# Kernel optimization log

Hardware: AMD Instinct MI355X
Metric: run time of the kernel (lower is better)

## Reference

```python
import jax, jax.numpy as jnp
import numpy as np

B, N, E = 8, 2000, 32000
LAT, STY, NF = 128, 64, 10
HEADS, HID = 4, 128
OUT = 3 + NF  # 13
EPS = 1e-5
SLOPE = 0.2


def _lin(k, fi, fo):
    return jax.random.normal(k, (fi, fo), dtype=jnp.float32) / np.sqrt(fi)


def setup_inputs() -> dict:
    key = jax.random.key(0)
    ks = jax.random.split(key, 32)
    inp = {
        'z': jax.random.normal(ks[0], (B, LAT), dtype=jnp.float32),
        'template_x': jax.random.normal(ks[1], (N, NF), dtype=jnp.float32),
        'template_edge_index': jax.random.randint(ks[2], (2, E), 0, N, dtype=jnp.int32),
        # style MLP
        'mlp_w1': _lin(ks[3], LAT, 256), 'mlp_b1': jnp.zeros((256,), jnp.float32),
        'mlp_w2': _lin(ks[4], 256, 512), 'mlp_b2': jnp.zeros((512,), jnp.float32),
        'mlp_w3': _lin(ks[5], 512, STY), 'mlp_b3': jnp.zeros((STY,), jnp.float32),
        # GAT1: in = NF + STY = 74 -> heads*HID = 512, concat
        'gat1_w': _lin(ks[6], NF + STY, HEADS * HID),
        'gat1_as': jax.random.normal(ks[7], (HEADS, HID), jnp.float32) * 0.1,
        'gat1_ad': jax.random.normal(ks[8], (HEADS, HID), jnp.float32) * 0.1,
        'gat1_b': jnp.zeros((HEADS * HID,), jnp.float32),
        'ln1_g': jnp.ones((HEADS * HID,), jnp.float32), 'ln1_b': jnp.zeros((HEADS * HID,), jnp.float32),
        # GAT2: 512 -> 512, concat
        'gat2_w': _lin(ks[9], HEADS * HID, HEADS * HID),
        'gat2_as': jax.random.normal(ks[10], (HEADS, HID), jnp.float32) * 0.1,
        'gat2_ad': jax.random.normal(ks[11], (HEADS, HID), jnp.float32) * 0.1,
        'gat2_b': jnp.zeros((HEADS * HID,), jnp.float32),
        'ln2_g': jnp.ones((HEADS * HID,), jnp.float32), 'ln2_b': jnp.zeros((HEADS * HID,), jnp.float32),
        # GAT3: 512 -> 13, 1 head, no concat
        'gat3_w': _lin(ks[12], HEADS * HID, OUT),
        'gat3_as': jax.random.normal(ks[13], (1, OUT), jnp.float32) * 0.1,
        'gat3_ad': jax.random.normal(ks[14], (1, OUT), jnp.float32) * 0.1,
        'gat3_b': jnp.zeros((OUT,), jnp.float32),
    }
    return inp


def gat_conv(x, src, dst, n_nodes, W, a_src, a_dst, bias, heads, out_ch, concat):
    # x: [NT, F_in]; per-head linear transform
    h = (x @ W).reshape(-1, heads, out_ch)              # [NT, H, C]
    als = jnp.sum(h * a_src[None], axis=-1)             # [NT, H]
    ald = jnp.sum(h * a_dst[None], axis=-1)             # [NT, H]
    logits = jax.nn.leaky_relu(als[src] + ald[dst], SLOPE)   # [E, H]
    # segment softmax over destination nodes (self-loops guarantee nonempty segments)
    mx = jax.ops.segment_max(logits, dst, num_segments=n_nodes)
    alpha = jnp.exp(logits - mx[dst])
    den = jax.ops.segment_sum(alpha, dst, num_segments=n_nodes)
    alpha = alpha / den[dst]                             # [E, H]
    msgs = h[src] * alpha[:, :, None]                    # [E, H, C]
    out = jax.ops.segment_sum(msgs, dst, num_segments=n_nodes)  # [NT, H, C]
    if concat:
        return out.reshape(n_nodes, heads * out_ch) + bias
    return out.mean(axis=1) + bias


def layer_norm(x, g, b):
    mu = jnp.mean(x, axis=-1, keepdims=True)
    var = jnp.mean((x - mu) ** 2, axis=-1, keepdims=True)
    return (x - mu) * jax.lax.rsqrt(var + EPS) * g + b


def reference(z, template_x, template_edge_index,
              mlp_w1, mlp_b1, mlp_w2, mlp_b2, mlp_w3, mlp_b3,
              gat1_w, gat1_as, gat1_ad, gat1_b, ln1_g, ln1_b,
              gat2_w, gat2_as, gat2_ad, gat2_b, ln2_g, ln2_b,
              gat3_w, gat3_as, gat3_ad, gat3_b):
    bsz = z.shape[0]
    n = template_x.shape[0]
    nt = bsz * n
    # batch the template graph: replicate nodes, offset edge indices per graph
    x = jnp.tile(template_x, (bsz, 1))                                  # [NT, NF]
    off = (jnp.arange(bsz, dtype=template_edge_index.dtype) * n)
    ei = (template_edge_index[:, None, :] + off[None, :, None]).reshape(2, -1)  # [2, B*E]
    loops = jnp.arange(nt, dtype=ei.dtype)
    src = jnp.concatenate([ei[0], loops])
    dst = jnp.concatenate([ei[1], loops])
    # style MLP
    s = jax.nn.leaky_relu(z @ mlp_w1 + mlp_b1, SLOPE)
    s = jax.nn.leaky_relu(s @ mlp_w2 + mlp_b2, SLOPE)
    s = s @ mlp_w3 + mlp_b3                                             # [B, STY]
    s_exp = jnp.repeat(s, n, axis=0)                                    # [NT, STY]
    H0 = jnp.concatenate([x, s_exp], axis=1)
    H1 = jax.nn.leaky_relu(gat_conv(H0, src, dst, nt, gat1_w, gat1_as, gat1_ad, gat1_b, HEADS, HID, True), SLOPE)
    H1n = layer_norm(H1, ln1_g, ln1_b)
    H2 = jax.nn.leaky_relu(gat_conv(H1n, src, dst, nt, gat2_w, gat2_as, gat2_ad, gat2_b, HEADS, HID, True), SLOPE)
    H2 = H2 + H1n
    H2n = layer_norm(H2, ln2_g, ln2_b)
    H_out = gat_conv(H2n, src, dst, nt, gat3_w, gat3_as, gat3_ad, gat3_b, 1, OUT, False)  # [NT, 13]
    delta_p = H_out[:, :3]
    delta_f = H_out[:, 3:]
    p_gen = x[:, :3] + delta_p
    X_gen = jnp.concatenate([p_gen, x[:, 3:] + delta_f[:, 3:]], axis=1)  # X[:, :3] overwritten by p_gen
    EF = p_gen[ei[1]] - p_gen[ei[0]]                                     # edge displacement vectors [B*E, 3]
    return X_gen, p_gen, EF
```

## Files before the change

kernel.cpp:

```cpp
#include <hip/hip_runtime.h>
#include <hip/hip_fp16.h>

constexpr int Bz = 8, Nn = 2000, Ee = 32000, NTOT = 16000;
constexpr int XG_OFF = 0, PG_OFF = 160000, EF_OFF = 208000;
#define SLOPE 0.2f
#define EPSL 1e-5f

typedef __attribute__((ext_vector_type(8))) _Float16 f16x8;
typedef __attribute__((ext_vector_type(4))) float float4v;

__device__ __forceinline__ float lrelu(float x) { return x > 0.f ? x : SLOPE * x; }

__device__ __forceinline__ unsigned short f2h(float x) {
  _Float16 hh = (_Float16)x;
  return *(unsigned short*)&hh;
}

__device__ __forceinline__ float wave_max(float v) {
  for (int o = 32; o; o >>= 1) v = fmaxf(v, __shfl_xor(v, o));
  return v;
}
__device__ __forceinline__ float wave_sum(float v) {
  for (int o = 32; o; o >>= 1) v += __shfl_xor(v, o);
  return v;
}

__global__ void hist_k(const int* __restrict__ tei, int* __restrict__ counts) {
  int j = blockIdx.x * 256 + threadIdx.x;
  if (j < Ee) atomicAdd(&counts[tei[Ee + j]], 1);
}

__global__ void scan_k(const int* __restrict__ counts, int* __restrict__ offs) {
  __shared__ int part[256];
  int t = threadIdx.x;
  int loc[8];
  int s = 0;
  for (int i = 0; i < 8; i++) {
    int idx = t * 8 + i;
    int c = (idx < Nn) ? counts[idx] : 0;
    loc[i] = s; s += c;
  }
  part[t] = s;
  __syncthreads();
  for (int o = 1; o < 256; o <<= 1) {
    int v = (t >= o) ? part[t - o] : 0;
    __syncthreads();
    part[t] += v;
    __syncthreads();
  }
  int excl = (t == 0) ? 0 : part[t - 1];
  for (int i = 0; i < 8; i++) {
    int idx = t * 8 + i;
    if (idx < Nn) offs[idx] = excl + loc[i];
  }
  if (t == 255) offs[Nn] = part[255];
}

__global__ void place_k(const int* __restrict__ tei, const int* __restrict__ offs,
                        int* __restrict__ cursor, int* __restrict__ colb) {
  int j = blockIdx.x * 256 + threadIdx.x;
  if (j < Ee) {
    int d = tei[Ee + j];
    int slot = offs[d] + atomicAdd(&cursor[d], 1);
    colb[slot] = tei[j];
  }
}

template <int K, int ACT>
__global__ __launch_bounds__(256) void lin_k(const float* __restrict__ x, const float* __restrict__ w,
                                             const float* __restrict__ bias, float* __restrict__ y,
                                             int O) {
  int gw = blockIdx.x * 4 + (threadIdx.x >> 6);
  int lane = threadIdx.x & 63;
  int bb = gw / O, o = gw - bb * O;
  float acc = 0.f;
#pragma unroll
  for (int k = lane; k < K; k += 64) acc += x[bb * K + k] * w[k * O + o];
  acc = wave_sum(acc);
  if (lane == 0) {
    if (bias) acc += bias[o];
    y[gw] = ACT ? lrelu(acc) : acc;
  }
}

__global__ __launch_bounds__(256) void w2bf_k(const float* __restrict__ W, unsigned short* __restrict__ Bt) {
  __shared__ float tile[32][33];
  int tx = threadIdx.x & 31, ty = threadIdx.x >> 5;
  int x0 = blockIdx.x * 32;
  int y0 = blockIdx.y * 32;
  for (int r = ty; r < 32; r += 8) tile[r][tx] = W[(y0 + r) * 512 + x0 + tx];
  __syncthreads();
  for (int r = ty; r < 32; r += 8) {
    unsigned short v = f2h(tile[tx][r]);
    size_t off = (size_t)(x0 + r) * 512 + (y0 + tx);
#pragma unroll
    for (int cp = 0; cp < 8; cp++) Bt[cp * 262144 + off] = v;
  }
}

__global__ void w3t_k(const float* __restrict__ W, unsigned short* __restrict__ W3t) {
  for (int idx = threadIdx.x; idx < 8192; idx += 256) {
    int col = idx >> 9, k = idx & 511;
    float v = (col < 13) ? W[k * 13 + col] : 0.f;
    W3t[idx] = f2h(v);
  }
}

__global__ __launch_bounds__(256) void tp16_k(const float* __restrict__ tx, const float* __restrict__ g1w,
                                              const float* __restrict__ a_s, const float* __restrict__ a_d,
                                              unsigned short* __restrict__ tp16, float* __restrict__ tpa,
                                              float* __restrict__ tpd) {
  int nl = blockIdx.x;
  int head = threadIdx.x >> 6, lane = threadIdx.x & 63;
  int c = head * 128 + 2 * lane;
  float t0 = 0.f, t1 = 0.f;
#pragma unroll
  for (int k = 0; k < 10; k++) {
    float xv = tx[nl * 10 + k];
    float2 wv = *(const float2*)&g1w[k * 512 + c];
    t0 += xv * wv.x; t1 += xv * wv.y;
  }
  ushort2 st; st.x = f2h(t0); st.y = f2h(t1);
  *(ushort2*)&tp16[(size_t)nl * 512 + c] = st;
  float2 av = *(const float2*)&a_s[c];
  float2 dv = *(const float2*)&a_d[c];
  float pa = wave_sum(t0 * av.x + t1 * av.y);
  float pd = wave_sum(t0 * dv.x + t1 * dv.y);
  if (lane == 0) { tpa[nl * 4 + head] = pa; tpd[nl * 4 + head] = pd; }
}

__global__ void pba_k(const float* __restrict__ pb, const float* __restrict__ a_s,
                      const float* __restrict__ a_d, float* __restrict__ pba, float* __restrict__ pbd) {
  int b = blockIdx.x >> 2, h = blockIdx.x & 3;
  int lane = threadIdx.x;
  int c = h * 128 + 2 * lane;
  float2 pv = *(const float2*)&pb[b * 512 + c];
  float2 av = *(const float2*)&a_s[c];
  float2 dv = *(const float2*)&a_d[c];
  float pa = wave_sum(pv.x * av.x + pv.y * av.y);
  float pd = wave_sum(pv.x * dv.x + pv.y * dv.y);
  if (lane == 0) { pba[b * 4 + h] = pa; pbd[b * 4 + h] = pd; }
}

__global__ __launch_bounds__(256) void agg1_k(const unsigned short* __restrict__ tp16,
                                              const float* __restrict__ tpa, const float* __restrict__ tpd,
                                              const float* __restrict__ pba, const float* __restrict__ pbd,
                                              const float* __restrict__ pb,
                                              const float* __restrict__ bias,
                                              const float* __restrict__ g, const float* __restrict__ beta,
                                              unsigned short* __restrict__ out,
                                              const int* __restrict__ offs, const int* __restrict__ colb) {
  int blk = blockIdx.x;
  int b = blk & 7, nl = blk >> 3;
  int n = b * Nn + nl;
  int w = threadIdx.x >> 6, lane = threadIdx.x & 63;
  int rs = offs[nl];
  int nit = offs[nl + 1] - rs + 1;
  float aldn = tpd[nl * 4 + w] + pbd[b * 4 + w];
  float pbsrc = pba[b * 4 + w];

  __shared__ unsigned int alpha_u[4][68];
  __shared__ int sgn[64];
  __shared__ float part[4][512];
  __shared__ float invs[4];
  __shared__ float red[8];
  __shared__ float bcs[2];

  __half2 acc2[4];
#pragma unroll
  for (int j = 0; j < 4; j++) acc2[j] = __float2half2_rn(0.f);

  const unsigned short* hbase = tp16 + lane * 8;
  int hd = lane >> 4;

  if (nit <= 64) {
    int se = nl;
    float logit = -3e38f;
    if (lane < nit) {
      se = (lane < nit - 1) ? colb[rs + lane] : nl;
      logit = lrelu(tpa[se * 4 + w] + pbsrc + aldn);
    }
    if (w == 0) sgn[lane] = se;
    float m = wave_max(logit);
    float raw = (lane < nit) ? __expf(logit - m) : 0.f;
    float den = wave_sum(raw);
    if (lane == 0) invs[w] = 1.f / den;
    __half2 a2 = __float2half2_rn(raw);
    alpha_u[w][lane] = *(unsigned int*)&a2;
    __syncthreads();
    int e = w;
    for (; e + 12 < nit; e += 16) {
      uint4 hv[4];
      unsigned int au[4];
#pragma unroll
      for (int i = 0; i < 4; i++) {
        int ei = e + i * 4;
        au[i] = alpha_u[hd][ei];
        hv[i] = *(const uint4*)(hbase + (size_t)sgn[ei] * 512);
      }
#pragma unroll
      for (int i = 0; i < 4; i++) {
        __half2 a2e = *(__half2*)&au[i];
        acc2[0] = __hfma2(a2e, *(__half2*)&hv[i].x, acc2[0]);
        acc2[1] = __hfma2(a2e, *(__half2*)&hv[i].y, acc2[1]);
        acc2[2] = __hfma2(a2e, *(__half2*)&hv[i].z, acc2[2]);
        acc2[3] = __hfma2(a2e, *(__half2*)&hv[i].w, acc2[3]);
      }
    }
    for (; e < nit; e += 4) {
      unsigned int au = alpha_u[hd][e];
      uint4 hv = *(const uint4*)(hbase + (size_t)sgn[e] * 512);
      __half2 a2e = *(__half2*)&au;
      acc2[0] = __hfma2(a2e, *(__half2*)&hv.x, acc2[0]);
      acc2[1] = __hfma2(a2e, *(__half2*)&hv.y, acc2[1]);
      acc2[2] = __hfma2(a2e, *(__half2*)&hv.z, acc2[2]);
      acc2[3] = __hfma2(a2e, *(__half2*)&hv.w, acc2[3]);
    }
  } else {
    float m = -3e38f;
    for (int i = lane; i < nit; i += 64) {
      int se = (i < nit - 1) ? colb[rs + i] : nl;
      m = fmaxf(m, lrelu(tpa[se * 4 + w] + pbsrc + aldn));
    }
    m = wave_max(m);
    float den = 0.f;
    for (int base = 0; base < nit; base += 64) {
      int cnt = min(64, nit - base);
      int se = nl;
      float raw = 0.f;
      if (lane < cnt) {
        int i = base + lane;
        se = (i < nit - 1) ? colb[rs + i] : nl;
        raw = __expf(lrelu(tpa[se * 4 + w] + pbsrc + aldn) - m);
      }
      if (w == 0) sgn[lane] = se;
      den += raw;
      __half2 a2 = __float2half2_rn(raw);
      alpha_u[w][lane] = *(unsigned int*)&a2;
      __syncthreads();
      for (int e = w; e < cnt; e += 4) {
        unsigned int au = alpha_u[hd][e];
        uint4 hv = *(const uint4*)(hbase + (size_t)sgn[e] * 512);
        __half2 a2e = *(__half2*)&au;
        acc2[0] = __hfma2(a2e, *(__half2*)&hv.x, acc2[0]);
        acc2[1] = __hfma2(a2e, *(__half2*)&hv.y, acc2[1]);
        acc2[2] = __hfma2(a2e, *(__half2*)&hv.z, acc2[2]);
        acc2[3] = __hfma2(a2e, *(__half2*)&hv.w, acc2[3]);
      }
      __syncthreads();
    }
    den = wave_sum(den);
    if (lane == 0) invs[w] = 1.f / den;
  }

  float fv[8];
#pragma unroll
  for (int j = 0; j < 4; j++) {
    float2 f2 = __half22float2(acc2[j]);
    fv[2 * j] = f2.x; fv[2 * j + 1] = f2.y;
  }
  *(float4*)&part[w][lane * 8] = make_float4(fv[0], fv[1], fv[2], fv[3]);
  *(float4*)&part[w][lane * 8 + 4] = make_float4(fv[4], fv[5], fv[6], fv[7]);
  __syncthreads();

  int c = 2 * (int)threadIdx.x;
  float inv = invs[c >> 7];
  float s0 = part[0][c] + part[1][c] + part[2][c] + part[3][c];
  float s1 = part[0][c + 1] + part[1][c + 1] + part[2][c + 1] + part[3][c + 1];
  float2 pv = *(const float2*)&pb[b * 512 + c];
  float v0 = lrelu(s0 * inv + pv.x + bias[c]);
  float v1 = lrelu(s1 * inv + pv.y + bias[c + 1]);
  float p1 = wave_sum(v0 + v1);
  float p2 = wave_sum(v0 * v0 + v1 * v1);
  if (lane == 0) { red[w] = p1; red[4 + w] = p2; }
  __syncthreads();
  if (threadIdx.x == 0) {
    float s1r = red[0] + red[1] + red[2] + red[3];
    float s2r = red[4] + red[5] + red[6] + red[7];
    float mu = s1r * (1.f / 512.f);
    float var = s2r * (1.f / 512.f) - mu * mu;
    bcs[0] = mu;
    bcs[1] = rsqrtf(var + EPSL);
  }
  __syncthreads();
  float mu = bcs[0], rstd = bcs[1];
  float o0 = (v0 - mu) * rstd * g[c] + beta[c];
  float o1 = (v1 - mu) * rstd * g[c + 1] + beta[c + 1];
  ushort2 st; st.x = f2h(o0); st.y = f2h(o1);
  *(ushort2*)&out[(size_t)n * 512 + c] = st;
}

__global__ __launch_bounds__(256) void agg_k(const unsigned short* __restrict__ h,
                                             const float* __restrict__ als, const float* __restrict__ ald,
                                             const float* __restrict__ bias,
                                             const float* __restrict__ g, const float* __restrict__ beta,
                                             const unsigned short* __restrict__ resid,
                                             unsigned short* __restrict__ out,
                                             const int* __restrict__ offs, const int* __restrict__ colb) {
  int blk = blockIdx.x;
  int b = blk & 7, nl = blk >> 3;
  int n = b * Nn + nl;
  int w = threadIdx.x >> 6, lane = threadIdx.x & 63;
  int rs = offs[nl];
  int nit = offs[nl + 1] - rs + 1;
  float aldn = ald[n * 4 + w];

  __shared__ unsigned int alpha_u[4][68];
  __shared__ int sgn[64];
  __shared__ float part[4][512];
  __shared__ float invs[4];
  __shared__ float red[8];
  __shared__ float bcs[2];

  __half2 acc2[4];
#pragma unroll
  for (int j = 0; j < 4; j++) acc2[j] = __float2half2_rn(0.f);

  const unsigned short* hbase = h + lane * 8;
  int hd = lane >> 4;

  if (nit <= 64) {
    int sg = n;
    float logit = -3e38f;
    if (lane < nit) {
      sg = (lane < nit - 1) ? colb[rs + lane] + b * Nn : n;
      logit = lrelu(als[sg * 4 + w] + aldn);
    }
    if (w == 0) sgn[lane] = sg;
    float m = wave_max(logit);
    float raw = (lane < nit) ? __expf(logit - m) : 0.f;
    float den = wave_sum(raw);
    if (lane == 0) invs[w] = 1.f / den;
    __half2 a2 = __float2half2_rn(raw);
    alpha_u[w][lane] = *(unsigned int*)&a2;
    __syncthreads();
    int e = w;
    for (; e + 12 < nit; e += 16) {
      uint4 hv[4];
      unsigned int au[4];
#pragma unroll
      for (int i = 0; i < 4; i++) {
        int ei = e + i * 4;
        au[i] = alpha_u[hd][ei];
        hv[i] = *(const uint4*)(hbase + (size_t)sgn[ei] * 512);
      }
#pragma unroll
      for (int i = 0; i < 4; i++) {
        __half2 a2e = *(__half2*)&au[i];
        acc2[0] = __hfma2(a2e, *(__half2*)&hv[i].x, acc2[0]);
        acc2[1] = __hfma2(a2e, *(__half2*)&hv[i].y, acc2[1]);
        acc2[2] = __hfma2(a2e, *(__half2*)&hv[i].z, acc2[2]);
        acc2[3] = __hfma2(a2e, *(__half2*)&hv[i].w, acc2[3]);
      }
    }
    for (; e < nit; e += 4) {
      unsigned int au = alpha_u[hd][e];
      uint4 hv = *(const uint4*)(hbase + (size_t)sgn[e] * 512);
      __half2 a2e = *(__half2*)&au;
      acc2[0] = __hfma2(a2e, *(__half2*)&hv.x, acc2[0]);
      acc2[1] = __hfma2(a2e, *(__half2*)&hv.y, acc2[1]);
      acc2[2] = __hfma2(a2e, *(__half2*)&hv.z, acc2[2]);
      acc2[3] = __hfma2(a2e, *(__half2*)&hv.w, acc2[3]);
    }
  } else {
    float m = -3e38f;
    for (int i = lane; i < nit; i += 64) {
      int sg = (i < nit - 1) ? colb[rs + i] + b * Nn : n;
      m = fmaxf(m, lrelu(als[sg * 4 + w] + aldn));
    }
    m = wave_max(m);
    float den = 0.f;
    for (int base = 0; base < nit; base += 64) {
      int cnt = min(64, nit - base);
      int sg = n;
      float raw = 0.f;
      if (lane < cnt) {
        int i = base + lane;
        sg = (i < nit - 1) ? colb[rs + i] + b * Nn : n;
        raw = __expf(lrelu(als[sg * 4 + w] + aldn) - m);
      }
      if (w == 0) sgn[lane] = sg;
      den += raw;
      __half2 a2 = __float2half2_rn(raw);
      alpha_u[w][lane] = *(unsigned int*)&a2;
      __syncthreads();
      for (int e = w; e < cnt; e += 4) {
        unsigned int au = alpha_u[hd][e];
        uint4 hv = *(const uint4*)(hbase + (size_t)sgn[e] * 512);
        __half2 a2e = *(__half2*)&au;
        acc2[0] = __hfma2(a2e, *(__half2*)&hv.x, acc2[0]);
        acc2[1] = __hfma2(a2e, *(__half2*)&hv.y, acc2[1]);
        acc2[2] = __hfma2(a2e, *(__half2*)&hv.z, acc2[2]);
        acc2[3] = __hfma2(a2e, *(__half2*)&hv.w, acc2[3]);
      }
      __syncthreads();
    }
    den = wave_sum(den);
    if (lane == 0) invs[w] = 1.f / den;
  }

  float fv[8];
#pragma unroll
  for (int j = 0; j < 4; j++) {
    float2 f2 = __half22float2(acc2[j]);
    fv[2 * j] = f2.x; fv[2 * j + 1] = f2.y;
  }
  *(float4*)&part[w][lane * 8] = make_float4(fv[0], fv[1], fv[2], fv[3]);
  *(float4*)&part[w][lane * 8 + 4] = make_float4(fv[4], fv[5], fv[6], fv[7]);
  __syncthreads();

  int c = 2 * (int)threadIdx.x;
  float inv = invs[c >> 7];
  float s0 = part[0][c] + part[1][c] + part[2][c] + part[3][c];
  float s1 = part[0][c + 1] + part[1][c + 1] + part[2][c + 1] + part[3][c + 1];
  float v0 = lrelu(s0 * inv + bias[c]);
  float v1 = lrelu(s1 * inv + bias[c + 1]);
  unsigned int rv = *(const unsigned int*)&resid[(size_t)n * 512 + c];
  __half2 rh = *(__half2*)&rv;
  float2 rf = __half22float2(rh);
  v0 += rf.x; v1 += rf.y;
  float p1 = wave_sum(v0 + v1);
  float p2 = wave_sum(v0 * v0 + v1 * v1);
  if (lane == 0) { red[w] = p1; red[4 + w] = p2; }
  __syncthreads();
  if (threadIdx.x == 0) {
    float s1r = red[0] + red[1] + red[2] + red[3];
    float s2r = red[4] + red[5] + red[6] + red[7];
    float mu = s1r * (1.f / 512.f);
    float var = s2r * (1.f / 512.f) - mu * mu;
    bcs[0] = mu;
    bcs[1] = rsqrtf(var + EPSL);
  }
  __syncthreads();
  float mu = bcs[0], rstd = bcs[1];
  float o0 = (v0 - mu) * rstd * g[c] + beta[c];
  float o1 = (v1 - mu) * rstd * g[c + 1] + beta[c + 1];
  ushort2 st; st.x = f2h(o0); st.y = f2h(o1);
  *(ushort2*)&out[(size_t)n * 512 + c] = st;
}

__global__ __launch_bounds__(512) void gemm2_k(const unsigned short* __restrict__ A,
                                               const unsigned short* __restrict__ Bt,
                                               unsigned short* __restrict__ C,
                                               const float* __restrict__ As, const float* __restrict__ Ad,
                                               float* __restrict__ als2, float* __restrict__ ald2) {
  __shared__ char smem[73728];
  char* sAc = smem;
  char* sBc = smem + 8192;
  int t = threadIdx.x;
  int lane = t & 63, w = t >> 6;
  int wm = w >> 2, wn = w & 3;
  int blk = blockIdx.x;
  int b = blk & 7, i = blk >> 3;
  int rows = min(64, Nn - i * 64);
  int m0 = b * Nn + i * 64;
  const unsigned short* Bl = Bt + (size_t)b * 262144;

  float4v acc[2][8];
#pragma unroll
  for (int q = 0; q < 2; q++)
#pragma unroll
    for (int j = 0; j < 8; j++) acc[q][j] = (float4v){0.f, 0.f, 0.f, 0.f};

  int arow = t >> 3, aklin = (t & 7) * 16;
  int asw = arow * 128 + (aklin ^ ((arow & 7) << 4));
  int arow_c = m0 + min(arow, rows - 1);
  int brow[8], bklin[8], bsw[8];
#pragma unroll
  for (int q = 0; q < 8; q++) {
    int slot = q * 512 + t;
    brow[q] = slot >> 3;
    bklin[q] = (slot & 7) * 16;
    bsw[q] = brow[q] * 128 + (bklin[q] ^ ((brow[q] & 7) << 4));
  }

  uint4 va = *(const uint4*)((const char*)A + (size_t)arow_c * 1024 + aklin);
  uint4 vb[8];
#pragma unroll
  for (int q = 0; q < 8; q++)
    vb[q] = *(const uint4*)((const char*)Bl + (size_t)brow[q] * 1024 + bklin[q]);

  int r_a = wm * 32 + (lane & 15);
  int r_b = wn * 128 + (lane & 15);
  int kbb = (lane >> 4) * 16;
  int sw = ((lane & 15) & 7) << 4;

  for (int k0 = 0; k0 < 512; k0 += 64) {
    if (k0) __syncthreads();
    *(uint4*)(sAc + asw) = va;
#pragma unroll
    for (int q = 0; q < 8; q++) *(uint4*)(sBc + bsw[q]) = vb[q];
    __syncthreads();
    if (k0 + 64 < 512) {
      va = *(const uint4*)((const char*)A + (size_t)arow_c * 1024 + (k0 + 64) * 2 + aklin);
#pragma unroll
      for (int q = 0; q < 8; q++)
        vb[q] = *(const uint4*)((const char*)Bl + (size_t)brow[q] * 1024 + (k0 + 64) * 2 + bklin[q]);
    }
#pragma unroll
    for (int ksub = 0; ksub < 2; ksub++) {
      f16x8 af[2], bg[8];
#pragma unroll
      for (int m = 0; m < 2; m++)
        af[m] = *(const f16x8*)(sAc + (r_a + m * 16) * 128 + ((ksub * 64 + kbb) ^ sw));
#pragma unroll
      for (int nn = 0; nn < 8; nn++)
        bg[nn] = *(const f16x8*)(sBc + (r_b + nn * 16) * 128 + ((ksub * 64 + kbb) ^ sw));
#pragma unroll
      for (int m = 0; m < 2; m++)
#pragma unroll
        for (int nn = 0; nn < 8; nn++)
          acc[m][nn] = __builtin_amdgcn_mfma_f32_16x16x32_f16(af[m], bg[nn], acc[m][nn], 0, 0, 0);
    }
  }

  {
    float asv[8], adv[8];
#pragma unroll
    for (int nn = 0; nn < 8; nn++) {
      asv[nn] = As[wn * 128 + nn * 16 + (lane & 15)];
      adv[nn] = Ad[wn * 128 + nn * 16 + (lane & 15)];
    }
#pragma unroll
    for (int m = 0; m < 2; m++) {
#pragma unroll
      for (int r = 0; r < 4; r++) {
        float pa = 0.f, pd = 0.f;
#pragma unroll
        for (int nn = 0; nn < 8; nn++) { pa += acc[m][nn][r] * asv[nn]; pd += acc[m][nn][r] * adv[nn]; }
        for (int o = 1; o < 16; o <<= 1) { pa += __shfl_xor(pa, o); pd += __shfl_xor(pd, o); }
        int lrow = wm * 32 + (lane >> 4) * 4 + m * 16 + r;
        if ((lane & 15) == 0 && lrow < rows) {
          als2[(m0 + lrow) * 4 + wn] = pa;
          ald2[(m0 + lrow) * 4 + wn] = pd;
        }
      }
    }
  }

  __syncthreads();
  unsigned short* sC = (unsigned short*)smem;
  int rbase = wm * 32 + (lane >> 4) * 4;
  int cbase = wn * 128 + (lane & 15);
#pragma unroll
  for (int m = 0; m < 2; m++)
#pragma unroll
    for (int nn = 0; nn < 8; nn++)
#pragma unroll
      for (int r = 0; r < 4; r++)
        sC[(rbase + m * 16 + r) * 520 + cbase + nn * 16] = f2h(acc[m][nn][r]);
  __syncthreads();
#pragma unroll
  for (int p = 0; p < 8; p++) {
    int row = p * 8 + (t >> 6);
    if (row < rows) {
      int co = (t & 63) * 8;
      uint4 v = *(const uint4*)&sC[row * 520 + co];
      *(uint4*)&C[(size_t)(m0 + row) * 512 + co] = v;
    }
  }
}

__global__ __launch_bounds__(256) void gemm3_k(const unsigned short* __restrict__ H,
                                               const unsigned short* __restrict__ W3t,
                                               const float* __restrict__ as3, const float* __restrict__ ad3,
                                               float* __restrict__ h3, float* __restrict__ als3,
                                               float* __restrict__ ald3) {
  int w = threadIdx.x >> 6, l = threadIdx.x & 63;
  int blk = blockIdx.x;
  int b = blk & 7, i = blk >> 3;
  int base = i * 64 + w * 16;
  int r16 = l & 15, g4 = l >> 4;
  int lrow_ld = min(base + r16, Nn - 1);
  float4v acc = (float4v){0.f, 0.f, 0.f, 0.f};
  const unsigned short* ha = H + (size_t)(b * Nn + lrow_ld) * 512 + g4 * 8;
  const unsigned short* wb = W3t + (size_t)r16 * 512 + g4 * 8;
#pragma unroll
  for (int kk = 0; kk < 16; kk++) {
    f16x8 a = *(const f16x8*)(ha + kk * 32);
    f16x8 bfr = *(const f16x8*)(wb + kk * 32);
    acc = __builtin_amdgcn_mfma_f32_16x16x32_f16(a, bfr, acc, 0, 0, 0);
  }
  int col = r16;
  float asv = (col < 13) ? as3[col] : 0.f;
  float adv = (col < 13) ? ad3[col] : 0.f;
#pragma unroll
  for (int r = 0; r < 4; r++) {
    float v = acc[r];
    int lrow = base + g4 * 4 + r;
    if (lrow < Nn) {
      int row = b * Nn + lrow;
      if (col < 13) h3[row * 13 + col] = v;
      float sa = v * asv, sd = v * adv;
      for (int o = 1; o < 16; o <<= 1) { sa += __shfl_xor(sa, o); sd += __shfl_xor(sd, o); }
      if (col == 0) { als3[row] = sa; ald3[row] = sd; }
    }
  }
}

__global__ __launch_bounds__(64) void agg3_k(const float* __restrict__ h3, const float* __restrict__ als3,
                                             const float* __restrict__ ald3, const float* __restrict__ b3,
                                             const float* __restrict__ tx, const int* __restrict__ offs,
                                             const int* __restrict__ colb, float* __restrict__ dout) {
  int blk = blockIdx.x, lane = threadIdx.x;
  int b = blk & 7, nl = blk >> 3;
  int n = b * Nn + nl;
  int rs = offs[nl], deg = offs[nl + 1] - rs;
  float aldn = ald3[n];
  float sl = lrelu(als3[n] + aldn);
  float a = 0.f, inv;
  if (deg <= 64) {
    int sgl = 0; float logit = -1e30f;
    if (lane < deg) { sgl = colb[rs + lane] + b * Nn; logit = lrelu(als3[sgl] + aldn); }
    float m = wave_max(fmaxf(logit, sl));
    float raw = (lane < deg) ? __expf(logit - m) : 0.f;
    float es = __expf(sl - m);
    inv = 1.f / (wave_sum(raw) + es);
    if (lane < 13) a = es * h3[n * 13 + lane];
    for (int e = 0; e < deg; e++) {
      float w = __shfl(raw, e);
      int sg = __shfl(sgl, e);
      if (lane < 13) a += w * h3[sg * 13 + lane];
    }
  } else {
    float m = sl;
    for (int e = lane; e < deg; e += 64) {
      int sg = colb[rs + e] + b * Nn;
      m = fmaxf(m, lrelu(als3[sg] + aldn));
    }
    m = wave_max(m);
    float es = __expf(sl - m);
    float den = (lane == 0) ? es : 0.f;
    if (lane < 13) a = es * h3[n * 13 + lane];
    for (int base = 0; base < deg; base += 64) {
      int cnt = min(64, deg - base);
      int sgl = 0; float raw = 0.f;
      if (lane < cnt) {
        sgl = colb[rs + base + lane] + b * Nn;
        raw = __expf(lrelu(als3[sgl] + aldn) - m);
      }
      den += raw;
      for (int e = 0; e < cnt; e++) {
        float w = __shfl(raw, e);
        int sg = __shfl(sgl, e);
        if (lane < 13) a += w * h3[sg * 13 + lane];
      }
    }
    inv = 1.f / wave_sum(den);
  }
  a *= inv;
  float hv = a + ((lane < 13) ? b3[lane] : 0.f);
  float txv = (lane < 10) ? tx[nl * 10 + lane] : 0.f;
  float pv = txv + hv;
  if (lane < 3) dout[PG_OFF + n * 3 + lane] = pv;
  float up = __shfl(hv, lane + 3);
  float xg = (lane < 3) ? pv : (txv + up);
  if (lane < 10) dout[XG_OFF + n * 10 + lane] = xg;
}

__global__ void ef_k(const int* __restrict__ tei, float* __restrict__ dout) {
  int blk = blockIdx.x;
  int b = blk & 7, i = blk >> 3;
  int j = i * 256 + threadIdx.x;
  int e = b * Ee + j;
  int sg = tei[j] + b * Nn;
  int dg = tei[Ee + j] + b * Nn;
  const float* pg = dout + PG_OFF;
  dout[EF_OFF + e * 3 + 0] = pg[dg * 3 + 0] - pg[sg * 3 + 0];
  dout[EF_OFF + e * 3 + 1] = pg[dg * 3 + 1] - pg[sg * 3 + 1];
  dout[EF_OFF + e * 3 + 2] = pg[dg * 3 + 2] - pg[sg * 3 + 2];
}

extern "C" void kernel_launch(void* const* d_in, const int* in_sizes, int n_in,
                              void* d_out, int out_size, void* d_ws, size_t ws_size,
                              hipStream_t stream) {
  const float* z = (const float*)d_in[0];
  const float* tx = (const float*)d_in[1];
  const int* tei = (const int*)d_in[2];
  const float* w1 = (const float*)d_in[3];
  const float* b1 = (const float*)d_in[4];
  const float* w2 = (const float*)d_in[5];
  const float* b2 = (const float*)d_in[6];
  const float* w3 = (const float*)d_in[7];
  const float* b3 = (const float*)d_in[8];
  const float* g1w = (const float*)d_in[9];
  const float* g1as = (const float*)d_in[10];
  const float* g1ad = (const float*)d_in[11];
  const float* g1b = (const float*)d_in[12];
  const float* ln1g = (const float*)d_in[13];
  const float* ln1b = (const float*)d_in[14];
  const float* g2w = (const float*)d_in[15];
  const float* g2as = (const float*)d_in[16];
  const float* g2ad = (const float*)d_in[17];
  const float* g2b = (const float*)d_in[18];
  const float* ln2g = (const float*)d_in[19];
  const float* ln2b = (const float*)d_in[20];
  const float* g3w = (const float*)d_in[21];
  const float* g3as = (const float*)d_in[22];
  const float* g3ad = (const float*)d_in[23];
  const float* g3b = (const float*)d_in[24];
  float* out = (float*)d_out;

  float* F = (float*)d_ws;
  float* pb_ = F + 0;
  float* l1_ = F + 8192;
  float* l2_ = F + 16384;
  float* s_ = F + 24576;
  float* pba_ = F + 30000;
  float* pbd_ = F + 30100;
  float* tpa_ = F + 100000;
  float* tpd_ = F + 164000;
  float* als2 = F + 228000;
  float* ald2 = F + 292000;
  float* als3 = F + 356000;
  float* ald3 = F + 372000;
  float* h3_ = F + 388000;
  unsigned short* U = (unsigned short*)(F + 600000);
  unsigned short* hA = U;
  unsigned short* hB = U + 8192000;
  unsigned short* Bt = U + 16384000;
  unsigned short* W3t = U + 18481152;
  unsigned short* tp16 = U + 18489344;
  int* I = (int*)(F + 12000000);
  int* counts = I;
  int* cursor = I + 2000;
  int* offs = I + 4000;
  int* colb = I + 6001;

  hipMemsetAsync(counts, 0, 4000 * sizeof(int), stream);
  hist_k<<<125, 256, 0, stream>>>(tei, counts);
  scan_k<<<1, 256, 0, stream>>>(counts, offs);
  place_k<<<125, 256, 0, stream>>>(tei, offs, cursor, colb);

  w2bf_k<<<dim3(16, 16), 256, 0, stream>>>(g2w, Bt);
  w3t_k<<<1, 256, 0, stream>>>(g3w, W3t);
  tp16_k<<<Nn, 256, 0, stream>>>(tx, g1w, g1as, g1ad, tp16, tpa_, tpd_);

  lin_k<128, 1><<<512, 256, 0, stream>>>(z, w1, b1, l1_, 256);
  lin_k<256, 1><<<1024, 256, 0, stream>>>(l1_, w2, b2, l2_, 512);
  lin_k<512, 0><<<128, 256, 0, stream>>>(l2_, w3, b3, s_, 64);
  lin_k<64, 0><<<1024, 256, 0, stream>>>(s_, g1w + 10 * 512, nullptr, pb_, 512);
  pba_k<<<32, 64, 0, stream>>>(pb_, g1as, g1ad, pba_, pbd_);

  agg1_k<<<NTOT, 256, 0, stream>>>(tp16, tpa_, tpd_, pba_, pbd_, pb_, g1b, ln1g, ln1b, hB, offs, colb);

  gemm2_k<<<256, 512, 0, stream>>>(hB, Bt, hA, g2as, g2ad, als2, ald2);
  agg_k<<<NTOT, 256, 0, stream>>>(hA, als2, ald2, g2b, ln2g, ln2b, hB, hB, offs, colb);

  gemm3_k<<<256, 256, 0, stream>>>(hB, W3t, g3as, g3ad, h3_, als3, ald3);
  agg3_k<<<NTOT, 64, 0, stream>>>(h3_, als3, ald3, g3b, tx, offs, colb, out);
  ef_k<<<1000, 256, 0, stream>>>(tei, out);
}
```

Baseline: 197.5 us.

## Fold GAT2 attention projections into agg1 and retile gemm2 as 128x64 tiles

```diff
diff --git a/kernel.cpp b/kernel.cpp
--- a/kernel.cpp
+++ b/kernel.cpp
@@ -104,6 +104,22 @@
     float v = (col < 13) ? W[k * 13 + col] : 0.f;
     W3t[idx] = f2h(v);
   }
+}
+
+__global__ __launch_bounds__(256) void wals_k(const float* __restrict__ g2w,
+                                              const float* __restrict__ a_s, const float* __restrict__ a_d,
+                                              float* __restrict__ wals, float* __restrict__ wald) {
+  int c = blockIdx.x;
+  int h = threadIdx.x >> 6, lane = threadIdx.x & 63;
+  float sa = 0.f, sd = 0.f;
+#pragma unroll
+  for (int j = lane; j < 128; j += 64) {
+    float wv = g2w[c * 512 + h * 128 + j];
+    sa += wv * a_s[h * 128 + j];
+    sd += wv * a_d[h * 128 + j];
+  }
+  sa = wave_sum(sa); sd = wave_sum(sd);
+  if (lane == 0) { wals[c * 4 + h] = sa; wald[c * 4 + h] = sd; }
 }
 
 __global__ __launch_bounds__(256) void tp16_k(const float* __restrict__ tx, const float* __restrict__ g1w,
@@ -148,7 +164,9 @@
                                               const float* __restrict__ pb,
                                               const float* __restrict__ bias,
                                               const float* __restrict__ g, const float* __restrict__ beta,
+                                              const float* __restrict__ wals, const float* __restrict__ wald,
                                               unsigned short* __restrict__ out,
+                                              float* __restrict__ als2, float* __restrict__ ald2,
                                               const int* __restrict__ offs, const int* __restrict__ colb) {
   int blk = blockIdx.x;
   int b = blk & 7, nl = blk >> 3;
@@ -164,6 +182,7 @@
   __shared__ float part[4][512];
   __shared__ float invs[4];
   __shared__ float red[8];
+  __shared__ float red2[4][8];
   __shared__ float bcs[2];
 
   __half2 acc2[4];
@@ -288,6 +307,29 @@
   float o1 = (v1 - mu) * rstd * g[c + 1] + beta[c + 1];
   ushort2 st; st.x = f2h(o0); st.y = f2h(o1);
   *(ushort2*)&out[(size_t)n * 512 + c] = st;
+
+  float4 wa0 = *(const float4*)&wals[c * 4];
+  float4 wa1 = *(const float4*)&wals[(c + 1) * 4];
+  float4 wd0 = *(const float4*)&wald[c * 4];
+  float4 wd1 = *(const float4*)&wald[(c + 1) * 4];
+  float sv[8];
+  sv[0] = o0 * wa0.x + o1 * wa1.x; sv[1] = o0 * wa0.y + o1 * wa1.y;
+  sv[2] = o0 * wa0.z + o1 * wa1.z; sv[3] = o0 * wa0.w + o1 * wa1.w;
+  sv[4] = o0 * wd0.x + o1 * wd1.x; sv[5] = o0 * wd0.y + o1 * wd1.y;
+  sv[6] = o0 * wd0.z + o1 * wd1.z; sv[7] = o0 * wd0.w + o1 * wd1.w;
+#pragma unroll
+  for (int j = 0; j < 8; j++) sv[j] = wave_sum(sv[j]);
+  if (lane == 0) {
+#pragma unroll
+    for (int j = 0; j < 8; j++) red2[w][j] = sv[j];
+  }
+  __syncthreads();
+  if (threadIdx.x < 8) {
+    int j = threadIdx.x;
+    float v = red2[0][j] + red2[1][j] + red2[2][j] + red2[3][j];
+    if (j < 4) als2[n * 4 + j] = v;
+    else ald2[n * 4 + (j - 4)] = v;
+  }
 }
 
 __global__ __launch_bounds__(256) void agg_k(const unsigned short* __restrict__ h,
@@ -439,125 +481,72 @@
   *(ushort2*)&out[(size_t)n * 512 + c] = st;
 }
 
-__global__ __launch_bounds__(512) void gemm2_k(const unsigned short* __restrict__ A,
+__global__ __launch_bounds__(256) void gemm2_k(const unsigned short* __restrict__ A,
                                                const unsigned short* __restrict__ Bt,
-                                               unsigned short* __restrict__ C,
-                                               const float* __restrict__ As, const float* __restrict__ Ad,
-                                               float* __restrict__ als2, float* __restrict__ ald2) {
-  __shared__ char smem[73728];
-  char* sAc = smem;
-  char* sBc = smem + 8192;
+                                               unsigned short* __restrict__ C) {
+  __shared__ unsigned short sB[64][520];
   int t = threadIdx.x;
   int lane = t & 63, w = t >> 6;
-  int wm = w >> 2, wn = w & 3;
-  int blk = blockIdx.x;
-  int b = blk & 7, i = blk >> 3;
-  int rows = min(64, Nn - i * 64);
-  int m0 = b * Nn + i * 64;
-  const unsigned short* Bl = Bt + (size_t)b * 262144;
-
-  float4v acc[2][8];
-#pragma unroll
-  for (int q = 0; q < 2; q++)
-#pragma unroll
-    for (int j = 0; j < 8; j++) acc[q][j] = (float4v){0.f, 0.f, 0.f, 0.f};
-
-  int arow = t >> 3, aklin = (t & 7) * 16;
-  int asw = arow * 128 + (aklin ^ ((arow & 7) << 4));
-  int arow_c = m0 + min(arow, rows - 1);
-  int brow[8], bklin[8], bsw[8];
-#pragma unroll
-  for (int q = 0; q < 8; q++) {
-    int slot = q * 512 + t;
-    brow[q] = slot >> 3;
-    bklin[q] = (slot & 7) * 16;
-    bsw[q] = brow[q] * 128 + (bklin[q] ^ ((brow[q] & 7) << 4));
-  }
-
-  uint4 va = *(const uint4*)((const char*)A + (size_t)arow_c * 1024 + aklin);
-  uint4 vb[8];
-#pragma unroll
-  for (int q = 0; q < 8; q++)
-    vb[q] = *(const uint4*)((const char*)Bl + (size_t)brow[q] * 1024 + bklin[q]);
-
-  int r_a = wm * 32 + (lane & 15);
-  int r_b = wn * 128 + (lane & 15);
-  int kbb = (lane >> 4) * 16;
-  int sw = ((lane & 15) & 7) << 4;
-
-  for (int k0 = 0; k0 < 512; k0 += 64) {
-    if (k0) __syncthreads();
-    *(uint4*)(sAc + asw) = va;
-#pragma unroll
-    for (int q = 0; q < 8; q++) *(uint4*)(sBc + bsw[q]) = vb[q];
-    __syncthreads();
-    if (k0 + 64 < 512) {
-      va = *(const uint4*)((const char*)A + (size_t)arow_c * 1024 + (k0 + 64) * 2 + aklin);
-#pragma unroll
-      for (int q = 0; q < 8; q++)
-        vb[q] = *(const uint4*)((const char*)Bl + (size_t)brow[q] * 1024 + (k0 + 64) * 2 + bklin[q]);
-    }
-#pragma unroll
-    for (int ksub = 0; ksub < 2; ksub++) {
-      f16x8 af[2], bg[8];
-#pragma unroll
-      for (int m = 0; m < 2; m++)
-        af[m] = *(const f16x8*)(sAc + (r_a + m * 16) * 128 + ((ksub * 64 + kbb) ^ sw));
-#pragma unroll
-      for (int nn = 0; nn < 8; nn++)
-        bg[nn] = *(const f16x8*)(sBc + (r_b + nn * 16) * 128 + ((ksub * 64 + kbb) ^ sw));
-#pragma unroll
-      for (int m = 0; m < 2; m++)
-#pragma unroll
-        for (int nn = 0; nn < 8; nn++)
-          acc[m][nn] = __builtin_amdgcn_mfma_f32_16x16x32_f16(af[m], bg[nn], acc[m][nn], 0, 0, 0);
-    }
-  }
-
-  {
-    float asv[8], adv[8];
-#pragma unroll
-    for (int nn = 0; nn < 8; nn++) {
-      asv[nn] = As[wn * 128 + nn * 16 + (lane & 15)];
-      adv[nn] = Ad[wn * 128 + nn * 16 + (lane & 15)];
-    }
-#pragma unroll
-    for (int m = 0; m < 2; m++) {
-#pragma unroll
-      for (int r = 0; r < 4; r++) {
-        float pa = 0.f, pd = 0.f;
-#pragma unroll
-        for (int nn = 0; nn < 8; nn++) { pa += acc[m][nn][r] * asv[nn]; pd += acc[m][nn][r] * adv[nn]; }
-        for (int o = 1; o < 16; o <<= 1) { pa += __shfl_xor(pa, o); pd += __shfl_xor(pd, o); }
-        int lrow = wm * 32 + (lane >> 4) * 4 + m * 16 + r;
-        if ((lane & 15) == 0 && lrow < rows) {
-          als2[(m0 + lrow) * 4 + wn] = pa;
-          ald2[(m0 + lrow) * 4 + wn] = pd;
-        }
-      }
-    }
-  }
-
-  __syncthreads();
-  unsigned short* sC = (unsigned short*)smem;
-  int rbase = wm * 32 + (lane >> 4) * 4;
-  int cbase = wn * 128 + (lane & 15);
+  int m0 = blockIdx.x * 128;
+  int n0 = blockIdx.y * 64;
+  const unsigned short* Bl = Bt + (size_t)((blockIdx.x + blockIdx.y * 125) & 7) * 262144;
+
+#pragma unroll
+  for (int q = 0; q < 16; q++) {
+    int slot = q * 256 + t;
+    int row = slot >> 6, c16 = (slot & 63) * 8;
+    *(uint4*)&sB[row][c16] = *(const uint4*)(Bl + (size_t)(n0 + row) * 512 + c16);
+  }
+  __syncthreads();
+
+  float4v acc[2][4];
 #pragma unroll
   for (int m = 0; m < 2; m++)
 #pragma unroll
-    for (int nn = 0; nn < 8; nn++)
+    for (int nn = 0; nn < 4; nn++) acc[m][nn] = (float4v){0.f, 0.f, 0.f, 0.f};
+
+  int r0 = m0 + w * 32 + (lane & 15);
+  int kb = (lane >> 4) * 8;
+  const unsigned short* a0p = A + (size_t)r0 * 512 + kb;
+  const unsigned short* a1p = A + (size_t)(r0 + 16) * 512 + kb;
+  int bc = lane & 15;
+
+#pragma unroll
+  for (int kf = 0; kf < 16; kf++) {
+    int k0 = kf * 32;
+    f16x8 af0 = *(const f16x8*)(a0p + k0);
+    f16x8 af1 = *(const f16x8*)(a1p + k0);
+    f16x8 bg0 = *(const f16x8*)&sB[bc][k0 + kb];
+    f16x8 bg1 = *(const f16x8*)&sB[16 + bc][k0 + kb];
+    f16x8 bg2 = *(const f16x8*)&sB[32 + bc][k0 + kb];
+    f16x8 bg3 = *(const f16x8*)&sB[48 + bc][k0 + kb];
+    acc[0][0] = __builtin_amdgcn_mfma_f32_16x16x32_f16(af0, bg0, acc[0][0], 0, 0, 0);
+    acc[0][1] = __builtin_amdgcn_mfma_f32_16x16x32_f16(af0, bg1, acc[0][1], 0, 0, 0);
+    acc[0][2] = __builtin_amdgcn_mfma_f32_16x16x32_f16(af0, bg2, acc[0][2], 0, 0, 0);
+    acc[0][3] = __builtin_amdgcn_mfma_f32_16x16x32_f16(af0, bg3, acc[0][3], 0, 0, 0);
+    acc[1][0] = __builtin_amdgcn_mfma_f32_16x16x32_f16(af1, bg0, acc[1][0], 0, 0, 0);
+    acc[1][1] = __builtin_amdgcn_mfma_f32_16x16x32_f16(af1, bg1, acc[1][1], 0, 0, 0);
+    acc[1][2] = __builtin_amdgcn_mfma_f32_16x16x32_f16(af1, bg2, acc[1][2], 0, 0, 0);
+    acc[1][3] = __builtin_amdgcn_mfma_f32_16x16x32_f16(af1, bg3, acc[1][3], 0, 0, 0);
+  }
+
+  __syncthreads();
+  unsigned short* sC = &sB[0][0];
+  int rb = w * 32 + (lane >> 4) * 4;
+#pragma unroll
+  for (int m = 0; m < 2; m++)
+#pragma unroll
+    for (int nn = 0; nn < 4; nn++)
 #pragma unroll
       for (int r = 0; r < 4; r++)
-        sC[(rbase + m * 16 + r) * 520 + cbase + nn * 16] = f2h(acc[m][nn][r]);
-  __syncthreads();
-#pragma unroll
-  for (int p = 0; p < 8; p++) {
-    int row = p * 8 + (t >> 6);
-    if (row < rows) {
-      int co = (t & 63) * 8;
-      uint4 v = *(const uint4*)&sC[row * 520 + co];
-      *(uint4*)&C[(size_t)(m0 + row) * 512 + co] = v;
-    }
+        sC[(rb + m * 16 + r) * 72 + bc + nn * 16] = f2h(acc[m][nn][r]);
+  __syncthreads();
+#pragma unroll
+  for (int p = 0; p < 4; p++) {
+    int row = p * 32 + (t >> 3);
+    int co = (t & 7) * 8;
+    uint4 v = *(const uint4*)&sC[row * 72 + co];
+    *(uint4*)&C[(size_t)(m0 + row) * 512 + n0 + co] = v;
   }
 }
 
@@ -708,6 +697,8 @@
   float* s_ = F + 24576;
   float* pba_ = F + 30000;
   float* pbd_ = F + 30100;
+  float* wals_ = F + 40000;
+  float* wald_ = F + 50000;
   float* tpa_ = F + 100000;
   float* tpd_ = F + 164000;
   float* als2 = F + 228000;
@@ -734,6 +725,7 @@
 
   w2bf_k<<<dim3(16, 16), 256, 0, stream>>>(g2w, Bt);
   w3t_k<<<1, 256, 0, stream>>>(g3w, W3t);
+  wals_k<<<512, 256, 0, stream>>>(g2w, g2as, g2ad, wals_, wald_);
   tp16_k<<<Nn, 256, 0, stream>>>(tx, g1w, g1as, g1ad, tp16, tpa_, tpd_);
 
   lin_k<128, 1><<<512, 256, 0, stream>>>(z, w1, b1, l1_, 256);
@@ -742,9 +734,10 @@
   lin_k<64, 0><<<1024, 256, 0, stream>>>(s_, g1w + 10 * 512, nullptr, pb_, 512);
   pba_k<<<32, 64, 0, stream>>>(pb_, g1as, g1ad, pba_, pbd_);
 
-  agg1_k<<<NTOT, 256, 0, stream>>>(tp16, tpa_, tpd_, pba_, pbd_, pb_, g1b, ln1g, ln1b, hB, offs, colb);
-
-  gemm2_k<<<256, 512, 0, stream>>>(hB, Bt, hA, g2as, g2ad, als2, ald2);
+  agg1_k<<<NTOT, 256, 0, stream>>>(tp16, tpa_, tpd_, pba_, pbd_, pb_, g1b, ln1g, ln1b,
+                                   wals_, wald_, hB, als2, ald2, offs, colb);
+
+  gemm2_k<<<dim3(125, 8), 256, 0, stream>>>(hB, Bt, hA);
   agg_k<<<NTOT, 256, 0, stream>>>(hA, als2, ald2, g2b, ln2g, ln2b, hB, hB, offs, colb);
 
   gemm3_k<<<256, 256, 0, stream>>>(hB, W3t, g3as, g3ad, h3_, als3, ald3);
```

Result: slower. 211.2 us (+6.9%).
